# Performance work log

Measured on AMD Instinct MI355X. Metric: run time of the kernel, lower is better.

## Reference

```python
import jax, jax.numpy as jnp
import numpy as np

B, T, E, H, K = 256, 512, 768, 100, 11
START, STOP = 9, 10
NEG = -1000.0


def setup_inputs() -> dict:
    key = jax.random.key(0)
    ks = jax.random.split(key, 12)
    s = 0.1
    Hd = H // 2  # per-direction hidden (bidirectional)
    trans = jax.random.normal(ks[9], (K, K), jnp.float32)
    trans = trans.at[:, START].set(NEG).at[STOP, :].set(NEG)
    return {
        "embeddings": jax.random.normal(ks[0], (B, T, E), jnp.float32),
        "input_mask": jnp.ones((B, T), jnp.int32),
        "W_ih_f": jax.random.normal(ks[1], (4 * Hd, E), jnp.float32) * s,
        "W_hh_f": jax.random.normal(ks[2], (4 * Hd, Hd), jnp.float32) * s,
        "b_f": jax.random.normal(ks[3], (4 * Hd,), jnp.float32) * s,
        "W_ih_b": jax.random.normal(ks[4], (4 * Hd, E), jnp.float32) * s,
        "W_hh_b": jax.random.normal(ks[5], (4 * Hd, Hd), jnp.float32) * s,
        "b_b": jax.random.normal(ks[6], (4 * Hd,), jnp.float32) * s,
        "W_out": jax.random.normal(ks[7], (K, H), jnp.float32) * s,
        "b_out": jax.random.normal(ks[8], (K,), jnp.float32) * s,
        "transitions": trans,
    }


def _lstm_dir(x, W_ih, W_hh, b, reverse):
    # x: [B, T, E] -> hidden states [B, T, Hd]; zero initial state.
    Bn = x.shape[0]
    Hd = W_hh.shape[1]

    def step(carry, xt):
        h, c = carry
        g = xt @ W_ih.T + h @ W_hh.T + b  # [B, 4*Hd], torch gate order i,f,g,o
        i, f, gg, o = jnp.split(g, 4, axis=-1)
        c = jax.nn.sigmoid(f) * c + jax.nn.sigmoid(i) * jnp.tanh(gg)
        h = jax.nn.sigmoid(o) * jnp.tanh(c)
        return (h, c), h

    init = (jnp.zeros((Bn, Hd), x.dtype), jnp.zeros((Bn, Hd), x.dtype))
    _, hs = jax.lax.scan(step, init, jnp.swapaxes(x, 0, 1), reverse=reverse)
    return jnp.swapaxes(hs, 0, 1)


def _emissions(embeddings, W_ih_f, W_hh_f, b_f, W_ih_b, W_hh_b, b_b, W_out, b_out):
    h_f = _lstm_dir(embeddings, W_ih_f, W_hh_f, b_f, reverse=False)
    h_b = _lstm_dir(embeddings, W_ih_b, W_hh_b, b_b, reverse=True)
    lstm_out = jnp.concatenate([h_f, h_b], axis=-1)  # [B, T, H]
    return lstm_out @ W_out.T + b_out  # [B, T, K]


def reference(embeddings, input_mask, W_ih_f, W_hh_f, b_f, W_ih_b, W_hh_b, b_b,
              W_out, b_out, transitions):
    logits = _emissions(embeddings, W_ih_f, W_hh_f, b_f, W_ih_b, W_hh_b, b_b,
                        W_out, b_out)  # [B, T, K]
    Bn = logits.shape[0]
    mask = (input_mask > 0)

    alpha0 = jnp.full((Bn, K), NEG, logits.dtype).at[:, START].set(0.0)
    idK = jnp.arange(K, dtype=jnp.int32)

    def step(alpha, inp):
        frame, m = inp  # frame [B,K], m [B] bool
        # smat[b, prev, cur] = alpha[b,prev] + frame[b,cur] + trans[prev,cur]
        smat = alpha[:, :, None] + frame[:, None, :] + transitions[None]
        bp = jnp.argmax(smat, axis=1).astype(jnp.int32)          # [B, K]
        new_alpha = jax.nn.logsumexp(smat, axis=1)               # [B, K]
        alpha = jnp.where(m[:, None], new_alpha, alpha)
        bp = jnp.where(m[:, None], bp, idK[None, :])
        return alpha, bp

    alpha_T, bps = jax.lax.scan(
        step, alpha0,
        (jnp.swapaxes(logits, 0, 1), jnp.swapaxes(mask, 0, 1)))  # bps [T,B,K]

    final = alpha_T + transitions[None, :, STOP]                 # [B, K]
    scores = jax.nn.logsumexp(final, axis=1)                     # [B]
    best = jnp.argmax(final, axis=1).astype(jnp.int32)           # [B]

    bidx = jnp.arange(Bn)

    def back(cur, bp_t):
        prev = bp_t[bidx, cur]
        return prev, prev

    # Original skips backtrace[0]; backtrack over positions 1..T-1.
    _, path_prefix = jax.lax.scan(back, best, bps[1:], reverse=True)  # [T-1, B]
    paths = jnp.concatenate(
        [jnp.swapaxes(path_prefix, 0, 1), best[:, None]], axis=1)     # [B, T]
    return scores, paths
```

## Files before the change

kernel.cpp:

```cpp
#include <hip/hip_runtime.h>
#include <math.h>


typedef _Float16 half8 __attribute__((ext_vector_type(8)));
typedef _Float16 half4 __attribute__((ext_vector_type(4)));
typedef float f32x4 __attribute__((ext_vector_type(4)));

__global__ __launch_bounds__(256) void k_gemm_split(
    const float* __restrict__ emb,
    const float* __restrict__ Wf,
    const float* __restrict__ Wb,
    float* __restrict__ xw)
{
    __shared__ _Float16 Ah[128 * 64];
    __shared__ _Float16 Al[128 * 64];
    __shared__ _Float16 Bh[80 * 64];
    __shared__ _Float16 Bl[80 * 64];

    const int bid = blockIdx.x;
    const int wg  = (bid & 7) * 640 + (bid >> 3);
    const int mt  = wg / 5;
    const int nb  = wg - mt * 5;
    const size_t m0 = (size_t)mt * 128;
    const int n0 = nb * 80;

    const int tid  = threadIdx.x;
    const int lane = tid & 63;
    const int w    = tid >> 6;
    const int grp  = lane >> 4;
    const int r16  = lane & 15;

    f32x4 acc[2][5];
    #pragma unroll
    for (int m = 0; m < 2; ++m)
        #pragma unroll
        for (int n = 0; n < 5; ++n) acc[m][n] = (f32x4){0.f, 0.f, 0.f, 0.f};

    for (int kt = 0; kt < 12; ++kt) {
        const int k0 = kt * 64;
        __syncthreads();

        #pragma unroll
        for (int j = 0; j < 8; ++j) {
            const int flat = j * 256 + tid;
            const int row  = flat >> 4;
            const int q    = flat & 15;
            const float4 v = *(const float4*)(emb + (m0 + row) * 768 + k0 + q * 4);
            half4 hv, lv;
            hv[0] = (_Float16)v.x; lv[0] = (_Float16)(v.x - (float)hv[0]);
            hv[1] = (_Float16)v.y; lv[1] = (_Float16)(v.y - (float)hv[1]);
            hv[2] = (_Float16)v.z; lv[2] = (_Float16)(v.z - (float)hv[2]);
            hv[3] = (_Float16)v.w; lv[3] = (_Float16)(v.w - (float)hv[3]);
            const int s    = (q >> 1) ^ (row & 7);
            const int addr = row * 64 + s * 8 + (q & 1) * 4;
            *(half4*)(Ah + addr) = hv;
            *(half4*)(Al + addr) = lv;
        }
        #pragma unroll
        for (int j = 0; j < 5; ++j) {
            const int flat = j * 256 + tid;
            const int row  = flat >> 4;
            const int q    = flat & 15;
            const int n    = n0 + row;
            const float* src = (n < 200) ? (Wf + (size_t)n * 768)
                                         : (Wb + (size_t)(n - 200) * 768);
            const float4 v = *(const float4*)(src + k0 + q * 4);
            half4 hv, lv;
            hv[0] = (_Float16)v.x; lv[0] = (_Float16)(v.x - (float)hv[0]);
            hv[1] = (_Float16)v.y; lv[1] = (_Float16)(v.y - (float)hv[1]);
            hv[2] = (_Float16)v.z; lv[2] = (_Float16)(v.z - (float)hv[2]);
            hv[3] = (_Float16)v.w; lv[3] = (_Float16)(v.w - (float)hv[3]);
            const int s    = (q >> 1) ^ (row & 7);
            const int addr = row * 64 + s * 8 + (q & 1) * 4;
            *(half4*)(Bh + addr) = hv;
            *(half4*)(Bl + addr) = lv;
        }
        __syncthreads();

        #pragma unroll
        for (int ks = 0; ks < 2; ++ks) {
            const int kslot = ks * 4 + grp;
            half8 ah[2], al[2], bh[5], bl[5];
            #pragma unroll
            for (int m = 0; m < 2; ++m) {
                const int row = w * 32 + m * 16 + r16;
                const int ad  = row * 64 + (kslot ^ (row & 7)) * 8;
                ah[m] = *(half8*)(Ah + ad);
                al[m] = *(half8*)(Al + ad);
            }
            #pragma unroll
            for (int n = 0; n < 5; ++n) {
                const int row = n * 16 + r16;
                const int ad  = row * 64 + (kslot ^ (row & 7)) * 8;
                bh[n] = *(half8*)(Bh + ad);
                bl[n] = *(half8*)(Bl + ad);
            }
            #pragma unroll
            for (int m = 0; m < 2; ++m)
                #pragma unroll
                for (int n = 0; n < 5; ++n) {
                    acc[m][n] = __builtin_amdgcn_mfma_f32_16x16x32_f16(ah[m], bh[n], acc[m][n], 0, 0, 0);
                    acc[m][n] = __builtin_amdgcn_mfma_f32_16x16x32_f16(ah[m], bl[n], acc[m][n], 0, 0, 0);
                    acc[m][n] = __builtin_amdgcn_mfma_f32_16x16x32_f16(al[m], bh[n], acc[m][n], 0, 0, 0);
                }
        }
    }

    #pragma unroll
    for (int m = 0; m < 2; ++m) {
        #pragma unroll
        for (int n = 0; n < 5; ++n) {
            #pragma unroll
            for (int i = 0; i < 4; ++i) {
                const size_t row = m0 + w * 32 + m * 16 + (lane >> 4) * 4 + i;
                const int    col = n0 + n * 16 + (lane & 15);
                xw[row * 400 + col] = acc[m][n][i];
            }
        }
    }
}

__global__ __launch_bounds__(256) void k_lstm(
    const float* __restrict__ xw,
    const float* __restrict__ Whh_f,
    const float* __restrict__ Whh_b,
    const float* __restrict__ bf_,
    const float* __restrict__ bb_,
    float* __restrict__ hout)
{
    const int b   = blockIdx.x >> 1;
    const int dir = blockIdx.x & 1;
    const int g   = threadIdx.x;

    __shared__ float h_s[52];
    __shared__ float g_s[200];

    const float* Whh  = dir ? Whh_b : Whh_f;
    const float* bias = dir ? bb_ : bf_;

    float w[52];
    float bg = 0.f;
    if (g < 200) {
        #pragma unroll
        for (int j = 0; j < 50; ++j) w[j] = Whh[g * 50 + j];
        w[50] = 0.f; w[51] = 0.f;
        bg = bias[g];
    } else {
        #pragma unroll
        for (int j = 0; j < 52; ++j) w[j] = 0.f;
    }

    if (g < 52) h_s[g] = 0.f;
    float c = 0.f;
    __syncthreads();

    const size_t base = (size_t)b * 512;

    float xv = 0.f;
    {
        int t0 = dir ? 511 : 0;
        if (g < 200) xv = xw[(base + t0) * 400 + dir * 200 + g];
    }

    for (int it = 0; it < 512; ++it) {
        const int t = dir ? (511 - it) : it;
        float xcur = xv;
        if (it + 1 < 512) {
            int tn = dir ? (510 - it) : (it + 1);
            if (g < 200) xv = xw[(base + tn) * 400 + dir * 200 + g];
        }

        float sum = bg + xcur;
        const float4* h4 = (const float4*)h_s;
        #pragma unroll
        for (int q = 0; q < 13; ++q) {
            float4 hv = h4[q];
            sum = fmaf(w[q * 4 + 0], hv.x, sum);
            sum = fmaf(w[q * 4 + 1], hv.y, sum);
            sum = fmaf(w[q * 4 + 2], hv.z, sum);
            sum = fmaf(w[q * 4 + 3], hv.w, sum);
        }
        if (g < 200) g_s[g] = sum;
        __syncthreads();

        if (g < 50) {
            float gi = g_s[g];
            float gf = g_s[g + 50];
            float gg = g_s[g + 100];
            float go = g_s[g + 150];
            float si = 1.f / (1.f + expf(-gi));
            float sf = 1.f / (1.f + expf(-gf));
            float so = 1.f / (1.f + expf(-go));
            c = sf * c + si * tanhf(gg);
            float h = so * tanhf(c);
            hout[(base + t) * 100 + dir * 50 + g] = h;
            h_s[g] = h;
        }
        __syncthreads();
    }
}

__global__ __launch_bounds__(256) void k_emis(
    const float* __restrict__ hout,
    const float* __restrict__ Wout,
    const float* __restrict__ bout,
    float* __restrict__ logits)
{
    __shared__ float Wl[1104];
    __shared__ float bl[11];
    const int tid = threadIdx.x;
    for (int i = tid; i < 1100; i += 256) Wl[i] = Wout[i];
    if (tid < 11) bl[tid] = bout[tid];
    __syncthreads();

    const size_t bt = (size_t)blockIdx.x * 256 + tid;
    const float4* h4 = (const float4*)(hout + bt * 100);
    float acc[11];
    #pragma unroll
    for (int k = 0; k < 11; ++k) acc[k] = bl[k];
    #pragma unroll
    for (int q = 0; q < 25; ++q) {
        float4 v = h4[q];
        #pragma unroll
        for (int k = 0; k < 11; ++k) {
            const float4 wv = *(const float4*)&Wl[k * 100 + q * 4];
            acc[k] = fmaf(v.x, wv.x, fmaf(v.y, wv.y, fmaf(v.z, wv.z, fmaf(v.w, wv.w, acc[k]))));
        }
    }
    #pragma unroll
    for (int k = 0; k < 11; ++k) logits[bt * 11 + k] = acc[k];
}

__global__ __launch_bounds__(64) void k_crf(
    const float* __restrict__ logits,
    const int* __restrict__ mask,
    const float* __restrict__ trans,
    float* __restrict__ scores,
    float* __restrict__ paths)
{
    const int b = blockIdx.x;
    const int lane = threadIdx.x;

    __shared__ float tr[121];
    __shared__ float al[12];
    __shared__ unsigned char bp[512][12];

    for (int i = lane; i < 121; i += 64) tr[i] = trans[i];
    if (lane < 12) al[lane] = (lane == 9) ? 0.f : -1000.f;
    __syncthreads();

    const size_t lbase = (size_t)b * 512;

    for (int t = 0; t < 512; ++t) {
        const int mt = mask[lbase + t];
        float na = 0.f; int amax = 0;
        if (lane < 11) {
            const float f = logits[(lbase + t) * 11 + lane];
            float vmax = -1e30f;
            float v[11];
            #pragma unroll
            for (int p = 0; p < 11; ++p) {
                float vv = (al[p] + f) + tr[p * 11 + lane];
                v[p] = vv;
                if (vv > vmax) { vmax = vv; amax = p; }
            }
            float s = 0.f;
            #pragma unroll
            for (int p = 0; p < 11; ++p) s += expf(v[p] - vmax);
            na = vmax + logf(s);
        }
        __syncthreads();
        if (lane < 11) {
            if (mt > 0) {
                al[lane] = na;
                bp[t][lane] = (unsigned char)amax;
            } else {
                bp[t][lane] = (unsigned char)lane;
            }
        }
        __syncthreads();
    }

    float fin = (lane < 11) ? (al[lane] + tr[lane * 11 + 10]) : -1e30f;
    float m = fin;
    int am = (lane < 11) ? lane : 1000;
    #pragma unroll
    for (int off = 8; off >= 1; off >>= 1) {
        float om = __shfl_xor(m, off, 16);
        int   oa = __shfl_xor(am, off, 16);
        if (om > m || (om == m && oa < am)) { m = om; am = oa; }
    }
    float s = (lane < 11) ? expf(fin - m) : 0.f;
    #pragma unroll
    for (int off = 8; off >= 1; off >>= 1) s += __shfl_xor(s, off, 16);

    if (lane == 0) {
        scores[b] = m + logf(s);
        int cur = am;
        paths[lbase + 511] = (float)cur;
        for (int t = 511; t >= 1; --t) {
            cur = bp[t][cur];
            paths[lbase + t - 1] = (float)cur;
        }
    }
}

extern "C" void kernel_launch(void* const* d_in, const int* in_sizes, int n_in,
                              void* d_out, int out_size, void* d_ws, size_t ws_size,
                              hipStream_t stream) {
    const float* emb   = (const float*)d_in[0];
    const int*   imask = (const int*)d_in[1];
    const float* Wihf  = (const float*)d_in[2];
    const float* Whhf  = (const float*)d_in[3];
    const float* bf_   = (const float*)d_in[4];
    const float* Wihb  = (const float*)d_in[5];
    const float* Whhb  = (const float*)d_in[6];
    const float* bb_   = (const float*)d_in[7];
    const float* Wout  = (const float*)d_in[8];
    const float* bout  = (const float*)d_in[9];
    const float* trans = (const float*)d_in[10];

    float* out = (float*)d_out;
    float* ws  = (float*)d_ws;
    float* xw     = ws;
    float* hout   = xw + (size_t)131072 * 400;
    float* logits = hout + (size_t)131072 * 100;

    k_gemm_split<<<5120, 256, 0, stream>>>(emb, Wihf, Wihb, xw);
    k_lstm<<<512, 256, 0, stream>>>(xw, Whhf, Whhb, bf_, bb_, hout);
    k_emis<<<512, 256, 0, stream>>>(hout, Wout, bout, logits);
    k_crf<<<256, 64, 0, stream>>>(logits, imask, trans, out, out + 256);
}
```

Measured before the change: 1.212 ms.

## Remap LSTM gates per wave with shuffles, double-buffer hidden state, fast activations

Reassigns LSTM recurrence threads so the four gates of each hidden unit sit in one wave, and combines them with lane shuffles instead of a shared-memory gate buffer. This removes one of the two block barriers per timestep. The hidden state is double-buffered, the input projection is prefetched four steps ahead, and the dot product is split into four accumulators to shorten the dependency chain. Sigmoid and tanh now use fast exp and reciprocal intrinsics, which may lose a little accuracy.

```diff
diff --git a/kernel.cpp b/kernel.cpp
--- a/kernel.cpp
+++ b/kernel.cpp
@@ -130,73 +130,89 @@
 {
     const int b   = blockIdx.x >> 1;
     const int dir = blockIdx.x & 1;
-    const int g   = threadIdx.x;
-
-    __shared__ float h_s[52];
-    __shared__ float g_s[200];
+    const int tid = threadIdx.x;
+    const int wv  = tid >> 6;
+    const int lane = tid & 63;
+    const int g4  = lane >> 4;
+    const int r16 = lane & 15;
+    const int u   = wv * 16 + r16;
+    const bool act = (u < 50);
+
+    __shared__ __align__(16) float hb[2][52];
 
     const float* Whh  = dir ? Whh_b : Whh_f;
     const float* bias = dir ? bb_ : bf_;
 
+    const int grow = g4 * 50 + u;
     float w[52];
     float bg = 0.f;
-    if (g < 200) {
-        #pragma unroll
-        for (int j = 0; j < 50; ++j) w[j] = Whh[g * 50 + j];
+    if (act) {
+        #pragma unroll
+        for (int j = 0; j < 50; ++j) w[j] = Whh[grow * 50 + j];
         w[50] = 0.f; w[51] = 0.f;
-        bg = bias[g];
+        bg = bias[grow];
     } else {
         #pragma unroll
         for (int j = 0; j < 52; ++j) w[j] = 0.f;
     }
 
-    if (g < 52) h_s[g] = 0.f;
+    if (tid < 104) ((float*)hb)[tid] = 0.f;
     float c = 0.f;
     __syncthreads();
 
     const size_t base = (size_t)b * 512;
-
-    float xv = 0.f;
-    {
-        int t0 = dir ? 511 : 0;
-        if (g < 200) xv = xw[(base + t0) * 400 + dir * 200 + g];
-    }
-
-    for (int it = 0; it < 512; ++it) {
-        const int t = dir ? (511 - it) : it;
-        float xcur = xv;
-        if (it + 1 < 512) {
-            int tn = dir ? (510 - it) : (it + 1);
-            if (g < 200) xv = xw[(base + tn) * 400 + dir * 200 + g];
-        }
-
-        float sum = bg + xcur;
-        const float4* h4 = (const float4*)h_s;
-        #pragma unroll
-        for (int q = 0; q < 13; ++q) {
-            float4 hv = h4[q];
-            sum = fmaf(w[q * 4 + 0], hv.x, sum);
-            sum = fmaf(w[q * 4 + 1], hv.y, sum);
-            sum = fmaf(w[q * 4 + 2], hv.z, sum);
-            sum = fmaf(w[q * 4 + 3], hv.w, sum);
-        }
-        if (g < 200) g_s[g] = sum;
-        __syncthreads();
-
-        if (g < 50) {
-            float gi = g_s[g];
-            float gf = g_s[g + 50];
-            float gg = g_s[g + 100];
-            float go = g_s[g + 150];
-            float si = 1.f / (1.f + expf(-gi));
-            float sf = 1.f / (1.f + expf(-gf));
-            float so = 1.f / (1.f + expf(-go));
-            c = sf * c + si * tanhf(gg);
-            float h = so * tanhf(c);
-            hout[(base + t) * 100 + dir * 50 + g] = h;
-            h_s[g] = h;
-        }
-        __syncthreads();
+    const int col = dir * 200 + grow;
+
+    float xv[4];
+    #pragma unroll
+    for (int k = 0; k < 4; ++k) {
+        const int tt = dir ? (511 - k) : k;
+        xv[k] = act ? xw[(base + tt) * 400 + col] : 0.f;
+    }
+
+    int cur = 0;
+    for (int it0 = 0; it0 < 512; it0 += 4) {
+        #pragma unroll
+        for (int k = 0; k < 4; ++k) {
+            const int it = it0 + k;
+            const int t  = dir ? (511 - it) : it;
+            const float xcur = xv[k];
+            if (it + 4 < 512) {
+                const int tn = dir ? (511 - (it + 4)) : (it + 4);
+                if (act) xv[k] = xw[(base + tn) * 400 + col];
+            }
+
+            const float4* h4 = (const float4*)(&hb[cur][0]);
+            float s0 = bg + xcur, s1 = 0.f, s2 = 0.f, s3 = 0.f;
+            #pragma unroll
+            for (int q = 0; q < 13; ++q) {
+                const float4 hv = h4[q];
+                s0 = fmaf(w[4 * q + 0], hv.x, s0);
+                s1 = fmaf(w[4 * q + 1], hv.y, s1);
+                s2 = fmaf(w[4 * q + 2], hv.z, s2);
+                s3 = fmaf(w[4 * q + 3], hv.w, s3);
+            }
+            const float sum = (s0 + s1) + (s2 + s3);
+
+            const float gi = __shfl(sum, r16);
+            const float gf = __shfl(sum, r16 + 16);
+            const float gg = __shfl(sum, r16 + 32);
+            const float go = __shfl(sum, r16 + 48);
+
+            if (g4 == 0 && act) {
+                const float si = __builtin_amdgcn_rcpf(1.f + __expf(-gi));
+                const float sf = __builtin_amdgcn_rcpf(1.f + __expf(-gf));
+                const float tg = 1.f - 2.f * __builtin_amdgcn_rcpf(__expf(2.f * gg) + 1.f);
+                c = sf * c + si * tg;
+                const float th = 1.f - 2.f * __builtin_amdgcn_rcpf(__expf(2.f * c) + 1.f);
+                const float so = __builtin_amdgcn_rcpf(1.f + __expf(-go));
+                const float h = so * th;
+                hout[(base + t) * 100 + dir * 50 + u] = h;
+                hb[cur ^ 1][u] = h;
+            }
+            __syncthreads();
+            cur ^= 1;
+        }
     }
 }
 
```

After: 1.250 ms. +3.1%, slower.

## Spread CRF Viterbi step across the wavefront with shuffles and prefetch

Applied to the files above, without the earlier changes.

The CRF forward recursion now computes the 121 score-matrix entries across all 64 lanes (two per lane), keeps alpha in registers exchanged via shuffles, and does the exponentials in parallel. Per-step __syncthreads are removed because a single wavefront is relied on for shared-memory ordering. Next-step logits and mask are prefetched to hide global load latency. This relies on the 64-thread block being exactly one wavefront, so the implicit lockstep makes the LDS writes visible without barriers.

```diff
diff --git a/kernel.cpp b/kernel.cpp
--- a/kernel.cpp
+++ b/kernel.cpp
@@ -231,7 +231,7 @@
     for (int k = 0; k < 11; ++k) logits[bt * 11 + k] = acc[k];
 }
 
-__global__ __launch_bounds__(64) void k_crf(
+__global__ __launch_bounds__(64, 1) void k_crf(
     const float* __restrict__ logits,
     const int* __restrict__ mask,
     const float* __restrict__ trans,
@@ -241,47 +241,78 @@
     const int b = blockIdx.x;
     const int lane = threadIdx.x;
 
-    __shared__ float tr[121];
-    __shared__ float al[12];
+    __shared__ float smat[11 * 12];
+    __shared__ float emat[11 * 12];
     __shared__ unsigned char bp[512][12];
 
-    for (int i = lane; i < 121; i += 64) tr[i] = trans[i];
-    if (lane < 12) al[lane] = (lane == 9) ? 0.f : -1000.f;
-    __syncthreads();
+    const int  pA = lane / 11, cA = lane - pA * 11;
+    const bool hasB = (lane < 57);
+    const int  iB = hasB ? (lane + 64) : 0;
+    const int  pB = iB / 11, cB = iB - pB * 11;
+
+    const float trA = trans[pA * 11 + cA];
+    const float trB = hasB ? trans[pB * 11 + cB] : 0.f;
+
+    float al_c = (lane == 9) ? 0.f : -1000.f;
 
     const size_t lbase = (size_t)b * 512;
 
+    float fA = logits[lbase * 11 + cA];
+    float fB = hasB ? logits[lbase * 11 + cB] : 0.f;
+    int   m_cur = mask[lbase];
+
     for (int t = 0; t < 512; ++t) {
-        const int mt = mask[lbase + t];
-        float na = 0.f; int amax = 0;
+        float fA_n = 0.f, fB_n = 0.f; int m_n = 1;
+        if (t + 1 < 512) {
+            fA_n = logits[(lbase + t + 1) * 11 + cA];
+            if (hasB) fB_n = logits[(lbase + t + 1) * 11 + cB];
+            m_n = mask[lbase + t + 1];
+        }
+
+        const float alA = __shfl(al_c, pA);
+        const float alB = __shfl(al_c, pB);
+        const float vvA = (alA + fA) + trA;
+        const float vvB = (alB + fB) + trB;
+        smat[cA * 12 + pA] = vvA;
+        if (hasB) smat[cB * 12 + pB] = vvB;
+
+        float vmax = -1e30f; int amax = 0;
         if (lane < 11) {
-            const float f = logits[(lbase + t) * 11 + lane];
-            float vmax = -1e30f;
             float v[11];
             #pragma unroll
+            for (int p = 0; p < 11; ++p) v[p] = smat[lane * 12 + p];
+            #pragma unroll
             for (int p = 0; p < 11; ++p) {
-                float vv = (al[p] + f) + tr[p * 11 + lane];
-                v[p] = vv;
-                if (vv > vmax) { vmax = vv; amax = p; }
-            }
+                if (v[p] > vmax) { vmax = v[p]; amax = p; }
+            }
+        }
+        const float vmA = __shfl(vmax, cA);
+        const float vmB = __shfl(vmax, cB);
+
+        const float eA = expf(vvA - vmA);
+        const float eB = expf(vvB - vmB);
+        emat[cA * 12 + pA] = eA;
+        if (hasB) emat[cB * 12 + pB] = eB;
+
+        if (lane < 11) {
+            float e[11];
+            #pragma unroll
+            for (int p = 0; p < 11; ++p) e[p] = emat[lane * 12 + p];
             float s = 0.f;
             #pragma unroll
-            for (int p = 0; p < 11; ++p) s += expf(v[p] - vmax);
-            na = vmax + logf(s);
-        }
-        __syncthreads();
-        if (lane < 11) {
-            if (mt > 0) {
-                al[lane] = na;
+            for (int p = 0; p < 11; ++p) s += e[p];
+            const float na = vmax + logf(s);
+            if (m_cur > 0) {
+                al_c = na;
                 bp[t][lane] = (unsigned char)amax;
             } else {
                 bp[t][lane] = (unsigned char)lane;
             }
         }
-        __syncthreads();
-    }
-
-    float fin = (lane < 11) ? (al[lane] + tr[lane * 11 + 10]) : -1e30f;
+        fA = fA_n; fB = fB_n; m_cur = m_n;
+    }
+
+    float fin = (lane < 11) ? (al_c + trans[lane * 11 + 10]) : -1e30f;
     float m = fin;
     int am = (lane < 11) ? lane : 1000;
     #pragma unroll
```

New measurement: 1.083 ms. 1.12x faster.

## Keep CRF forward state in registers with shuffles and prefetch next frame

Applied to the files above, without the earlier changes.

Rewrites the CRF forward recursion to hold alpha and the transition column in registers, broadcasting alpha across the wavefront with shuffles instead of shared memory plus two block barriers per step. The logsumexp is refactored to take the max over alpha only and use precomputed exp(transition) factors, with fast __expf/__logf intrinsics, and the next frame's logits and mask are prefetched one step ahead. This shortens the serial 512-step dependency chain; the change of logsumexp factoring and the fast intrinsics slightly alter numerics, and using the max over alpha alone could underflow when transition values are very negative.

```diff
diff --git a/kernel.cpp b/kernel.cpp
--- a/kernel.cpp
+++ b/kernel.cpp
@@ -231,7 +231,7 @@
     for (int k = 0; k < 11; ++k) logits[bt * 11 + k] = acc[k];
 }
 
-__global__ __launch_bounds__(64) void k_crf(
+__global__ __launch_bounds__(64, 1) void k_crf(
     const float* __restrict__ logits,
     const int* __restrict__ mask,
     const float* __restrict__ trans,
@@ -240,48 +240,71 @@
 {
     const int b = blockIdx.x;
     const int lane = threadIdx.x;
-
-    __shared__ float tr[121];
-    __shared__ float al[12];
+    const int lanec = (lane < 11) ? lane : 10;
+
     __shared__ unsigned char bp[512][12];
 
-    for (int i = lane; i < 121; i += 64) tr[i] = trans[i];
-    if (lane < 12) al[lane] = (lane == 9) ? 0.f : -1000.f;
-    __syncthreads();
+    float trc[11], E[11];
+    #pragma unroll
+    for (int p = 0; p < 11; ++p) {
+        trc[p] = trans[p * 11 + lanec];
+        E[p]   = expf(trc[p]);
+    }
+
+    float al_c = (lane == 9) ? 0.f : -1000.f;
 
     const size_t lbase = (size_t)b * 512;
 
+    float f_cur = logits[lbase * 11 + lanec];
+    int   m_cur = mask[lbase];
+
     for (int t = 0; t < 512; ++t) {
-        const int mt = mask[lbase + t];
-        float na = 0.f; int amax = 0;
+        float f_next = 0.f; int m_next = 1;
+        if (t + 1 < 512) {
+            f_next = logits[(lbase + t + 1) * 11 + lanec];
+            m_next = mask[lbase + t + 1];
+        }
+
+        float a[11];
+        #pragma unroll
+        for (int p = 0; p < 11; ++p) a[p] = __shfl(al_c, p);
+
+        float vmax = a[0] + trc[0]; int amax = 0;
+        #pragma unroll
+        for (int p = 1; p < 11; ++p) {
+            const float vp = a[p] + trc[p];
+            if (vp > vmax) { vmax = vp; amax = p; }
+        }
+
+        const float m01 = fmaxf(a[0], a[1]),  m23 = fmaxf(a[2], a[3]);
+        const float m45 = fmaxf(a[4], a[5]),  m67 = fmaxf(a[6], a[7]);
+        const float m89 = fmaxf(a[8], a[9]);
+        const float mA  = fmaxf(fmaxf(m01, m23), fmaxf(m45, m67));
+        const float M   = fmaxf(mA, fmaxf(m89, a[10]));
+
+        float e[11];
+        #pragma unroll
+        for (int p = 0; p < 11; ++p) e[p] = __expf(a[p] - M) * E[p];
+        const float s01 = e[0] + e[1], s23 = e[2] + e[3];
+        const float s45 = e[4] + e[5], s67 = e[6] + e[7];
+        const float s89 = e[8] + e[9];
+        const float S = ((s01 + s23) + (s45 + s67)) + (s89 + e[10]);
+
+        const float na = f_cur + (M + __logf(S));
+
         if (lane < 11) {
-            const float f = logits[(lbase + t) * 11 + lane];
-            float vmax = -1e30f;
-            float v[11];
-            #pragma unroll
-            for (int p = 0; p < 11; ++p) {
-                float vv = (al[p] + f) + tr[p * 11 + lane];
-                v[p] = vv;
-                if (vv > vmax) { vmax = vv; amax = p; }
-            }
-            float s = 0.f;
-            #pragma unroll
-            for (int p = 0; p < 11; ++p) s += expf(v[p] - vmax);
-            na = vmax + logf(s);
-        }
-        __syncthreads();
-        if (lane < 11) {
-            if (mt > 0) {
-                al[lane] = na;
+            if (m_cur > 0) {
+                al_c = na;
                 bp[t][lane] = (unsigned char)amax;
             } else {
                 bp[t][lane] = (unsigned char)lane;
             }
         }
-        __syncthreads();
-    }
-
-    float fin = (lane < 11) ? (al[lane] + tr[lane * 11 + 10]) : -1e30f;
+        f_cur = f_next;
+        m_cur = m_next;
+    }
+
+    float fin = (lane < 11) ? (al_c + trans[lane * 11 + 10]) : -1e30f;
     float m = fin;
     int am = (lane < 11) ? lane : 1000;
     #pragma unroll
```

After: 1.004 ms. 17.2% less time.
